# Performance work log

Measured on AMD Instinct MI355X. Metric: run time of the kernel, lower is better.

Reference implementation:

```python
import jax, jax.numpy as jnp
import numpy as np

N, E, L, S = 10000, 200000, 128, 10
NODE_IN, EDGE_IN = 29, 4  # vel_hist(15)+vel_mag(5)+bound(6)+force(3); rel_disp(3)+rel_dist(1)
EPS = 1e-5  # haiku LayerNorm default


def _mlp(x, params):
    # hk.nets.MLP([L]*num_mlp_layers + [out]) with relu activations
    for W, b in params[:-1]:
        x = jax.nn.relu(x @ W + b)
    W, b = params[-1]
    return x @ W + b


def _ln(x, s, o):
    m = jnp.mean(x, axis=-1, keepdims=True)
    v = jnp.mean(jnp.square(x - m), axis=-1, keepdims=True)
    return (x - m) * jax.lax.rsqrt(v + EPS) * s + o


def _init_mlp(key, dims, stack=None):
    Ws, bs = [], []
    for i in range(len(dims) - 1):
        key, k = jax.random.split(key)
        shp = (dims[i], dims[i + 1]) if stack is None else (stack, dims[i], dims[i + 1])
        Ws.append(jax.random.normal(k, shp, jnp.float32) / np.float32(np.sqrt(dims[i])))
        bshp = (dims[i + 1],) if stack is None else (stack, dims[i + 1])
        bs.append(jnp.zeros(bshp, jnp.float32))
    return Ws, bs


def setup_inputs() -> dict:
    key = jax.random.key(0)
    ks = jax.random.split(key, 16)
    inp = {
        'vel_hist': jax.random.normal(ks[0], (N, 15), jnp.float32),
        'vel_mag': jax.random.normal(ks[1], (N, 5), jnp.float32),
        'bound': jax.random.normal(ks[2], (N, 6), jnp.float32),
        'force': jax.random.normal(ks[3], (N, 3), jnp.float32),
        'rel_disp': jax.random.normal(ks[4], (E, 3), jnp.float32),
        'rel_dist': jax.random.normal(ks[5], (E, 1), jnp.float32),
        'senders': jax.random.randint(ks[6], (E,), 0, N, jnp.int32),
        'receivers': jax.random.randint(ks[7], (E,), 0, N, jnp.int32),
    }
    enW, enB = _init_mlp(ks[8], [NODE_IN, L, L, L])
    eeW, eeB = _init_mlp(ks[9], [EDGE_IN, L, L, L])
    peW, peB = _init_mlp(ks[10], [3 * L, L, L, L], stack=S)
    pnW, pnB = _init_mlp(ks[11], [2 * L, L, L, L], stack=S)
    deW, deB = _init_mlp(ks[12], [L, L, L, 3])
    for pre, (Ws, Bs) in [('en', (enW, enB)), ('ee', (eeW, eeB)), ('pe', (peW, peB)), ('pn', (pnW, pnB)), ('de', (deW, deB))]:
        for i in range(3):
            inp[f'{pre}_W{i}'] = Ws[i]
            inp[f'{pre}_b{i}'] = Bs[i]
    inp['en_s'] = jnp.ones((L,), jnp.float32); inp['en_o'] = jnp.zeros((L,), jnp.float32)
    inp['ee_s'] = jnp.ones((L,), jnp.float32); inp['ee_o'] = jnp.zeros((L,), jnp.float32)
    inp['pe_s'] = jnp.ones((S, L), jnp.float32); inp['pe_o'] = jnp.zeros((S, L), jnp.float32)
    inp['pn_s'] = jnp.ones((S, L), jnp.float32); inp['pn_o'] = jnp.zeros((S, L), jnp.float32)
    return inp


def reference(vel_hist, vel_mag, bound, force, rel_disp, rel_dist,
              en_W0, en_b0, en_W1, en_b1, en_W2, en_b2, en_s, en_o,
              ee_W0, ee_b0, ee_W1, ee_b1, ee_W2, ee_b2, ee_s, ee_o,
              pe_W0, pe_b0, pe_W1, pe_b1, pe_W2, pe_b2, pe_s, pe_o,
              pn_W0, pn_b0, pn_W1, pn_b1, pn_W2, pn_b2, pn_s, pn_o,
              de_W0, de_b0, de_W1, de_b1, de_W2, de_b2,
              senders, receivers):
    n = vel_hist.shape[0]
    # encoder
    nodes = _ln(_mlp(jnp.concatenate([vel_hist, vel_mag, bound, force], -1),
                     [(en_W0, en_b0), (en_W1, en_b1), (en_W2, en_b2)]), en_s, en_o)
    edges = _ln(_mlp(jnp.concatenate([rel_disp, rel_dist], -1),
                     [(ee_W0, ee_b0), (ee_W1, ee_b1), (ee_W2, ee_b2)]), ee_s, ee_o)

    # processor: S GraphNetwork blocks with residual adds (distinct params per step)
    def step(carry, p):
        nd, ed = carry
        (W0, b0, W1, b1, W2, b2, s, o, nW0, nb0, nW1, nb1, nW2, nb2, ns, no) = p
        e_in = jnp.concatenate([nd[senders], nd[receivers], ed], -1)  # [E, 3L]
        e_new = _ln(_mlp(e_in, [(W0, b0), (W1, b1), (W2, b2)]), s, o)
        aggr = jax.ops.segment_sum(e_new, receivers, num_segments=n)  # [N, L]
        n_new = _ln(_mlp(jnp.concatenate([nd, aggr], -1), [(nW0, nb0), (nW1, nb1), (nW2, nb2)]), ns, no)
        return (nd + n_new, ed + e_new), None

    (nodes, edges), _ = jax.lax.scan(
        step, (nodes, edges),
        (pe_W0, pe_b0, pe_W1, pe_b1, pe_W2, pe_b2, pe_s, pe_o,
         pn_W0, pn_b0, pn_W1, pn_b1, pn_W2, pn_b2, pn_s, pn_o))

    # decoder (no layer norm)
    return _mlp(nodes, [(de_W0, de_b0), (de_W1, de_b1), (de_W2, de_b2)])
```

## Files before the change

kernel.cpp:

```cpp
#include <hip/hip_runtime.h>

#define NN 10000
#define NE 200000
#define LDIM 128
#define PADB 136
#define NSTEP 10
#define LN_EPS 1e-5f

typedef unsigned short ushort_t;
typedef __attribute__((ext_vector_type(8))) short short8;
typedef __attribute__((ext_vector_type(4))) float f32x4;

#define MFMA16(a, b, c) __builtin_amdgcn_mfma_f32_16x16x32_bf16(a, b, c, 0, 0, 0)

__device__ __forceinline__ ushort_t f2bf(float f) {
  unsigned int u = __float_as_uint(f);
  return (ushort_t)((u + 0x7FFFu + ((u >> 16) & 1u)) >> 16);
}
__device__ __forceinline__ float bf2f(ushort_t h) {
  return __uint_as_float(((unsigned int)h) << 16);
}


#define STAGE_WT(WT, KTOT, K0)                                              \
  {                                                                         \
    const ushort_t* src_ = (WT) + (size_t)(t >> 1) * (KTOT) + (K0) + (t & 1) * 64; \
    ushort_t* dst_ = &Wbuf[(t >> 1) * PADB + (t & 1) * 64];                 \
    _Pragma("unroll")                                                       \
    for (int q_ = 0; q_ < 8; ++q_)                                          \
      *(uint4*)(dst_ + q_ * 8) = *(const uint4*)(src_ + q_ * 8);            \
  }

#define INIT_ACC(BG)                                                        \
  _Pragma("unroll")                                                         \
  for (int nt_ = 0; nt_ < 8; ++nt_) {                                       \
    float bv_ = (BG)[nt_ * 16 + lr];                                        \
    acc[0][nt_] = (f32x4){bv_, bv_, bv_, bv_};                              \
    acc[1][nt_] = acc[0][nt_];                                              \
  }

#define MFMA_K128()                                                         \
  _Pragma("unroll")                                                         \
  for (int ks_ = 0; ks_ < 4; ++ks_) {                                       \
    short8 a0_ = *(const short8*)&Abuf[(rw + lr) * PADB + ks_ * 32 + kg * 8];        \
    short8 a1_ = *(const short8*)&Abuf[(rw + 16 + lr) * PADB + ks_ * 32 + kg * 8];   \
    _Pragma("unroll")                                                       \
    for (int nt_ = 0; nt_ < 8; ++nt_) {                                     \
      short8 b_ = *(const short8*)&Wbuf[(nt_ * 16 + lr) * PADB + ks_ * 32 + kg * 8]; \
      acc[0][nt_] = MFMA16(a0_, b_, acc[0][nt_]);                           \
      acc[1][nt_] = MFMA16(a1_, b_, acc[1][nt_]);                           \
    }                                                                       \
  }

#define RELU_TO_ABUF()                                                      \
  _Pragma("unroll")                                                         \
  for (int mt_ = 0; mt_ < 2; ++mt_) {                                       \
    _Pragma("unroll")                                                       \
    for (int nt_ = 0; nt_ < 8; ++nt_) {                                     \
      _Pragma("unroll")                                                     \
      for (int i_ = 0; i_ < 4; ++i_) {                                      \
        int row_ = rw + 16 * mt_ + kg * 4 + i_;                             \
        Abuf[row_ * PADB + nt_ * 16 + lr] = f2bf(fmaxf(acc[mt_][nt_][i_], 0.f)); \
      }                                                                     \
    }                                                                       \
  }

#define LN_STATS2(MARR, RARR)                                               \
  float MARR[2][4], RARR[2][4];                                             \
  _Pragma("unroll")                                                         \
  for (int mt_ = 0; mt_ < 2; ++mt_) {                                       \
    _Pragma("unroll")                                                       \
    for (int i_ = 0; i_ < 4; ++i_) {                                        \
      float s_ = 0.f;                                                       \
      _Pragma("unroll")                                                     \
      for (int nt_ = 0; nt_ < 8; ++nt_) s_ += acc[mt_][nt_][i_];            \
      s_ += __shfl_xor(s_, 1); s_ += __shfl_xor(s_, 2);                     \
      s_ += __shfl_xor(s_, 4); s_ += __shfl_xor(s_, 8);                     \
      float m_ = s_ * (1.f / 128.f);                                        \
      float v_ = 0.f;                                                       \
      _Pragma("unroll")                                                     \
      for (int nt_ = 0; nt_ < 8; ++nt_) {                                   \
        float d_ = acc[mt_][nt_][i_] - m_; v_ = fmaf(d_, d_, v_);           \
      }                                                                     \
      v_ += __shfl_xor(v_, 1); v_ += __shfl_xor(v_, 2);                     \
      v_ += __shfl_xor(v_, 4); v_ += __shfl_xor(v_, 8);                     \
      MARR[mt_][i_] = m_;                                                   \
      RARR[mt_][i_] = rsqrtf(v_ * (1.f / 128.f) + LN_EPS);                  \
    }                                                                       \
  }

#define LN_TO_FBUF(FB)                                                      \
  _Pragma("unroll")                                                         \
  for (int mt_ = 0; mt_ < 2; ++mt_)                                         \
    _Pragma("unroll")                                                       \
    for (int i_ = 0; i_ < 4; ++i_) {                                        \
      int row_ = rw + 16 * mt_ + kg * 4 + i_;                               \
      _Pragma("unroll")                                                     \
      for (int nt_ = 0; nt_ < 8; ++nt_)                                     \
        (FB)[row_ * 132 + nt_ * 16 + lr] =                                  \
            (acc[mt_][nt_][i_] - lmean[mt_][i_]) * lrstd[mt_][i_] * sv[nt_] + ov[nt_]; \
    }

__global__ void k_prep_w(const float* __restrict__ src, ushort_t* __restrict__ dst,
                         int Ksrc, int Kdst, int N, int steps) {
  const size_t total = (size_t)steps * N * Kdst;
  for (size_t idx = (size_t)blockIdx.x * blockDim.x + threadIdx.x; idx < total;
       idx += (size_t)gridDim.x * blockDim.x) {
    int k = (int)(idx % Kdst);
    size_t tmp = idx / Kdst;
    int n = (int)(tmp % N);
    int s = (int)(tmp / N);
    float v = (k < Ksrc) ? src[((size_t)s * Ksrc + k) * N + n] : 0.f;
    dst[idx] = f2bf(v);
  }
}

__global__ void k_hist(const int* __restrict__ recv, int* __restrict__ cnt) {
  int e = blockIdx.x * 256 + threadIdx.x;
  if (e < NE) atomicAdd(&cnt[recv[e]], 1);
}

__global__ __launch_bounds__(256)
void k_scan(const int* __restrict__ cnt, int* __restrict__ row_start) {
  __shared__ int part[256];
  const int t = threadIdx.x;
  const int base = t * 40;
  int sum = 0;
  for (int i = 0; i < 40; ++i) {
    int b = base + i;
    if (b < NN) sum += cnt[b];
  }
  part[t] = sum;
  __syncthreads();
  for (int off = 1; off < 256; off <<= 1) {
    int v = part[t];
    int u = (t >= off) ? part[t - off] : 0;
    __syncthreads();
    part[t] = v + u;
    __syncthreads();
  }
  int run = (t == 0) ? 0 : part[t - 1];
  for (int i = 0; i < 40; ++i) {
    int b = base + i;
    if (b < NN) { row_start[b] = run; run += cnt[b]; }
  }
  if (t == 255) row_start[NN] = run;
}

__global__ void k_scatter(const int* __restrict__ send, const int* __restrict__ recv,
                          const int* __restrict__ row_start, int* __restrict__ cursor,
                          int* __restrict__ esrc, int* __restrict__ sSend,
                          int* __restrict__ sRecv) {
  int e = blockIdx.x * 256 + threadIdx.x;
  if (e >= NE) return;
  int r = recv[e];
  int pos = row_start[r] + atomicAdd(&cursor[r], 1);
  esrc[pos] = e;
  sSend[pos] = send[e];
  sRecv[pos] = r;
}

__global__ __launch_bounds__(256, 2)
void k_enc_node_m(const float* __restrict__ vh, const float* __restrict__ vm,
                  const float* __restrict__ bd, const float* __restrict__ fc,
                  const ushort_t* __restrict__ Wt0, const float* __restrict__ b0,
                  const ushort_t* __restrict__ Wt1, const float* __restrict__ b1,
                  const ushort_t* __restrict__ Wt2, const float* __restrict__ b2,
                  const float* __restrict__ lns, const float* __restrict__ lno,
                  float* __restrict__ nodes_f, ushort_t* __restrict__ nodes_bf) {
  __shared__ ushort_t Abuf[128 * PADB];
  __shared__ ushort_t Wbuf[128 * PADB];
  const int t = threadIdx.x;
  const int lane = t & 63, wid = t >> 6;
  const int lr = lane & 15, kg = lane >> 4;
  const int rw = wid * 32;
  const int n0 = blockIdx.x * 128;

  for (int idx = t; idx < 128 * 32; idx += 256) {
    int r = idx >> 5, k = idx & 31;
    int ng = n0 + r;
    float v = 0.f;
    if (ng < NN) {
      if (k < 15)      v = vh[(size_t)ng * 15 + k];
      else if (k < 20) v = vm[(size_t)ng * 5 + (k - 15)];
      else if (k < 26) v = bd[(size_t)ng * 6 + (k - 20)];
      else if (k < 29) v = fc[(size_t)ng * 3 + (k - 26)];
    }
    Abuf[r * PADB + k] = f2bf(v);
  }
  {
    const ushort_t* src = Wt0 + (t >> 1) * 32 + (t & 1) * 16;
    ushort_t* dst = &Wbuf[(t >> 1) * PADB + (t & 1) * 16];
    *(uint4*)dst = *(const uint4*)src;
    *(uint4*)(dst + 8) = *(const uint4*)(src + 8);
  }
  f32x4 acc[2][8];
  INIT_ACC(b0)
  __syncthreads();
  {
    short8 a0_ = *(const short8*)&Abuf[(rw + lr) * PADB + kg * 8];
    short8 a1_ = *(const short8*)&Abuf[(rw + 16 + lr) * PADB + kg * 8];
#pragma unroll
    for (int nt_ = 0; nt_ < 8; ++nt_) {
      short8 b_ = *(const short8*)&Wbuf[(nt_ * 16 + lr) * PADB + kg * 8];
      acc[0][nt_] = MFMA16(a0_, b_, acc[0][nt_]);
      acc[1][nt_] = MFMA16(a1_, b_, acc[1][nt_]);
    }
  }
  __syncthreads();
  RELU_TO_ABUF()
  INIT_ACC(b1)
  STAGE_WT(Wt1, 128, 0)
  __syncthreads();
  MFMA_K128()
  __syncthreads();
  RELU_TO_ABUF()
  INIT_ACC(b2)
  STAGE_WT(Wt2, 128, 0)
  __syncthreads();
  MFMA_K128()

  LN_STATS2(lmean, lrstd)
  float sv[8], ov[8];
#pragma unroll
  for (int nt = 0; nt < 8; ++nt) { sv[nt] = lns[nt * 16 + lr]; ov[nt] = lno[nt * 16 + lr]; }
#pragma unroll
  for (int mt = 0; mt < 2; ++mt)
#pragma unroll
    for (int i = 0; i < 4; ++i) {
      int row = rw + 16 * mt + kg * 4 + i;
      int ng = n0 + row;
      if (ng < NN) {
#pragma unroll
        for (int nt = 0; nt < 8; ++nt) {
          float o = (acc[mt][nt][i] - lmean[mt][i]) * lrstd[mt][i] * sv[nt] + ov[nt];
          size_t idx = (size_t)ng * LDIM + nt * 16 + lr;
          nodes_f[idx] = o;
          nodes_bf[idx] = f2bf(o);
        }
      }
    }
}

__global__ __launch_bounds__(256, 2)
void k_enc_edge_m(const float* __restrict__ rel_disp, const float* __restrict__ rel_dist,
                  const int* __restrict__ esrc,
                  const ushort_t* __restrict__ Wt0, const float* __restrict__ b0,
                  const ushort_t* __restrict__ Wt1, const float* __restrict__ b1,
                  const ushort_t* __restrict__ Wt2, const float* __restrict__ b2,
                  const float* __restrict__ lns, const float* __restrict__ lno,
                  float* __restrict__ edges_f) {
  __shared__ ushort_t smem[2 * 128 * PADB];
  __shared__ int eidx[128];
  ushort_t* Abuf = smem;
  ushort_t* Wbuf = smem + 128 * PADB;
  const int t = threadIdx.x;
  const int lane = t & 63, wid = t >> 6;
  const int lr = lane & 15, kg = lane >> 4;
  const int rw = wid * 32;
  const int e0 = blockIdx.x * 128;

  if (t < 128) eidx[t] = (e0 + t < NE) ? esrc[e0 + t] : 0;
  __syncthreads();

  for (int idx = t; idx < 128 * 32; idx += 256) {
    int r = idx >> 5, k = idx & 31;
    float v = 0.f;
    if (e0 + r < NE) {
      int eo = eidx[r];
      if (k < 3)       v = rel_disp[(size_t)eo * 3 + k];
      else if (k == 3) v = rel_dist[eo];
    }
    Abuf[r * PADB + k] = f2bf(v);
  }
  {
    const ushort_t* src = Wt0 + (t >> 1) * 32 + (t & 1) * 16;
    ushort_t* dst = &Wbuf[(t >> 1) * PADB + (t & 1) * 16];
    *(uint4*)dst = *(const uint4*)src;
    *(uint4*)(dst + 8) = *(const uint4*)(src + 8);
  }
  f32x4 acc[2][8];
  INIT_ACC(b0)
  __syncthreads();
  {
    short8 a0_ = *(const short8*)&Abuf[(rw + lr) * PADB + kg * 8];
    short8 a1_ = *(const short8*)&Abuf[(rw + 16 + lr) * PADB + kg * 8];
#pragma unroll
    for (int nt_ = 0; nt_ < 8; ++nt_) {
      short8 b_ = *(const short8*)&Wbuf[(nt_ * 16 + lr) * PADB + kg * 8];
      acc[0][nt_] = MFMA16(a0_, b_, acc[0][nt_]);
      acc[1][nt_] = MFMA16(a1_, b_, acc[1][nt_]);
    }
  }
  __syncthreads();
  RELU_TO_ABUF()
  INIT_ACC(b1)
  STAGE_WT(Wt1, 128, 0)
  __syncthreads();
  MFMA_K128()
  __syncthreads();
  RELU_TO_ABUF()
  INIT_ACC(b2)
  STAGE_WT(Wt2, 128, 0)
  __syncthreads();
  MFMA_K128()

  LN_STATS2(lmean, lrstd)
  float sv[8], ov[8];
#pragma unroll
  for (int nt = 0; nt < 8; ++nt) { sv[nt] = lns[nt * 16 + lr]; ov[nt] = lno[nt * 16 + lr]; }

  float* fbuf = (float*)smem;
  __syncthreads();
  LN_TO_FBUF(fbuf)
  __syncthreads();
#pragma unroll
  for (int q = 0; q < 16; ++q) {
    int F = wid * 4096 + q * 256 + lane * 4;
    int row = F >> 7, col = F & 127;
    if (e0 + row < NE) {
      float4 v = *(const float4*)&fbuf[row * 132 + col];
      *(float4*)&edges_f[(size_t)e0 * LDIM + F] = v;
    }
  }
}

__global__ __launch_bounds__(256, 2)
void k_proc_edge_m(const ushort_t* __restrict__ nodes_bf, float* __restrict__ edges_f,
                   float* __restrict__ aggr,
                   const int* __restrict__ sSend, const int* __restrict__ sRecv,
                   const ushort_t* __restrict__ Wt0, const float* __restrict__ b0,
                   const ushort_t* __restrict__ Wt1, const float* __restrict__ b1,
                   const ushort_t* __restrict__ Wt2, const float* __restrict__ b2,
                   const float* __restrict__ lns, const float* __restrict__ lno) {
  __shared__ ushort_t smem[2 * 128 * PADB];
  __shared__ int sidx[128], ridx[128];
  ushort_t* Abuf = smem;
  ushort_t* Wbuf = smem + 128 * PADB;
  const int t = threadIdx.x;
  const int lane = t & 63, wid = t >> 6;
  const int lr = lane & 15, kg = lane >> 4;
  const int rw = wid * 32;
  const int e0 = blockIdx.x * 128;

  if (t < 128) sidx[t] = (e0 + t < NE) ? sSend[e0 + t] : 0;
  else         ridx[t - 128] = (e0 + t - 128 < NE) ? sRecv[e0 + t - 128] : -1;

  f32x4 acc[2][8];
  float4 eold[16];
  INIT_ACC(b0)
  __syncthreads();

#pragma unroll
  for (int seg = 0; seg < 3; ++seg) {
    if (seg) __syncthreads();
    if (seg < 2) {
      const int r = t >> 1, h = t & 1;
      const int srow = (seg == 0) ? sidx[r] : ((ridx[r] < 0) ? 0 : ridx[r]);
      const ushort_t* src = nodes_bf + (size_t)srow * LDIM + h * 64;
      ushort_t* dst = &Abuf[r * PADB + h * 64];
#pragma unroll
      for (int q = 0; q < 8; ++q)
        *(uint4*)(dst + q * 8) = *(const uint4*)(src + q * 8);
    } else {
#pragma unroll
      for (int q = 0; q < 16; ++q) {
        int F = wid * 4096 + q * 256 + lane * 4;
        int row = F >> 7, col = F & 127;
        float4 v;
        if (e0 + row < NE) v = *(const float4*)&edges_f[(size_t)e0 * LDIM + F];
        else { v.x = v.y = v.z = v.w = 0.f; }
        eold[q] = v;
        ushort4 hv;
        hv.x = f2bf(v.x); hv.y = f2bf(v.y); hv.z = f2bf(v.z); hv.w = f2bf(v.w);
        *(ushort4*)&Abuf[row * PADB + col] = hv;
      }
    }
    STAGE_WT(Wt0, 384, seg * 128)
    __syncthreads();
    MFMA_K128()
  }
  __syncthreads();
  RELU_TO_ABUF()
  INIT_ACC(b1)
  STAGE_WT(Wt1, 128, 0)
  __syncthreads();
  MFMA_K128()
  __syncthreads();
  RELU_TO_ABUF()
  INIT_ACC(b2)
  STAGE_WT(Wt2, 128, 0)
  __syncthreads();
  MFMA_K128()

  LN_STATS2(lmean, lrstd)
  float sv[8], ov[8];
#pragma unroll
  for (int nt = 0; nt < 8; ++nt) { sv[nt] = lns[nt * 16 + lr]; ov[nt] = lno[nt * 16 + lr]; }

  float* fbuf = (float*)smem;
  __syncthreads();
  LN_TO_FBUF(fbuf)
  __syncthreads();

#pragma unroll
  for (int q = 0; q < 16; ++q) {
    int F = wid * 4096 + q * 256 + lane * 4;
    int row = F >> 7, col = F & 127;
    if (e0 + row < NE) {
      float4 nv = *(const float4*)&fbuf[row * 132 + col];
      nv.x += eold[q].x; nv.y += eold[q].y; nv.z += eold[q].z; nv.w += eold[q].w;
      *(float4*)&edges_f[(size_t)e0 * LDIM + F] = nv;
    }
  }

  {
    const int c = t & 127;
    const int half = t >> 7;
    const int r0 = half * 64, r1 = r0 + 64;
    float run = 0.f;
    int cur = ridx[r0];
    for (int r = r0; r < r1; ++r) {
      int rid = ridx[r];
      if (rid != cur) {
        if (cur >= 0) atomicAdd(&aggr[(size_t)cur * LDIM + c], run);
        run = 0.f;
        cur = rid;
      }
      run += fbuf[r * 132 + c];
    }
    if (cur >= 0) atomicAdd(&aggr[(size_t)cur * LDIM + c], run);
  }
}

__global__ __launch_bounds__(256, 2)
void k_proc_node_m(float* __restrict__ nodes_f, ushort_t* __restrict__ nodes_bf,
                   const float* __restrict__ aggr,
                   const ushort_t* __restrict__ Wt0, const float* __restrict__ b0,
                   const ushort_t* __restrict__ Wt1, const float* __restrict__ b1,
                   const ushort_t* __restrict__ Wt2, const float* __restrict__ b2,
                   const float* __restrict__ lns, const float* __restrict__ lno) {
  __shared__ ushort_t Abuf[128 * PADB];
  __shared__ ushort_t Wbuf[128 * PADB];
  const int t = threadIdx.x;
  const int lane = t & 63, wid = t >> 6;
  const int lr = lane & 15, kg = lane >> 4;
  const int rw = wid * 32;
  const int n0 = blockIdx.x * 128;

  f32x4 acc[2][8];
  INIT_ACC(b0)

#pragma unroll
  for (int seg = 0; seg < 2; ++seg) {
    if (seg) __syncthreads();
    {
      const int r = t >> 1, h = t & 1;
      const int ng = n0 + r;
      ushort_t* dst = &Abuf[r * PADB + h * 64];
      if (ng < NN) {
        if (seg == 0) {
          const ushort_t* src = nodes_bf + (size_t)ng * LDIM + h * 64;
#pragma unroll
          for (int q = 0; q < 8; ++q)
            *(uint4*)(dst + q * 8) = *(const uint4*)(src + q * 8);
        } else {
          const float* src = aggr + (size_t)ng * LDIM + h * 64;
#pragma unroll
          for (int q = 0; q < 16; ++q) {
            float4 fv = *(const float4*)(src + q * 4);
            ushort4 hv;
            hv.x = f2bf(fv.x); hv.y = f2bf(fv.y); hv.z = f2bf(fv.z); hv.w = f2bf(fv.w);
            *(ushort4*)(dst + q * 4) = hv;
          }
        }
      } else {
        uint4 z; z.x = z.y = z.z = z.w = 0u;
#pragma unroll
        for (int q = 0; q < 8; ++q) *(uint4*)(dst + q * 8) = z;
      }
    }
    STAGE_WT(Wt0, 256, seg * 128)
    __syncthreads();
    MFMA_K128()
  }
  __syncthreads();
  RELU_TO_ABUF()
  INIT_ACC(b1)
  STAGE_WT(Wt1, 128, 0)
  __syncthreads();
  MFMA_K128()
  __syncthreads();
  RELU_TO_ABUF()
  INIT_ACC(b2)
  STAGE_WT(Wt2, 128, 0)
  __syncthreads();
  MFMA_K128()

  LN_STATS2(lmean, lrstd)
  float sv[8], ov[8];
#pragma unroll
  for (int nt = 0; nt < 8; ++nt) { sv[nt] = lns[nt * 16 + lr]; ov[nt] = lno[nt * 16 + lr]; }
#pragma unroll
  for (int mt = 0; mt < 2; ++mt)
#pragma unroll
    for (int i = 0; i < 4; ++i) {
      int row = rw + 16 * mt + kg * 4 + i;
      int ng = n0 + row;
      if (ng < NN) {
#pragma unroll
        for (int nt = 0; nt < 8; ++nt) {
          float o = (acc[mt][nt][i] - lmean[mt][i]) * lrstd[mt][i] * sv[nt] + ov[nt];
          size_t idx = (size_t)ng * LDIM + nt * 16 + lr;
          float nv = nodes_f[idx] + o;
          nodes_f[idx] = nv;
          nodes_bf[idx] = f2bf(nv);
        }
      }
    }
}

__global__ __launch_bounds__(256, 2)
void k_dec_m(const ushort_t* __restrict__ nodes_bf,
             const ushort_t* __restrict__ Wt0, const float* __restrict__ b0,
             const ushort_t* __restrict__ Wt1, const float* __restrict__ b1,
             const float* __restrict__ W2f, const float* __restrict__ b2,
             float* __restrict__ out) {
  __shared__ ushort_t Abuf[128 * PADB];
  __shared__ ushort_t Wbuf[128 * PADB];
  const int t = threadIdx.x;
  const int lane = t & 63, wid = t >> 6;
  const int lr = lane & 15, kg = lane >> 4;
  const int rw = wid * 32;
  const int n0 = blockIdx.x * 128;

  {
    const int r = t >> 1, h = t & 1;
    const int ng = n0 + r;
    ushort_t* dst = &Abuf[r * PADB + h * 64];
    if (ng < NN) {
      const ushort_t* src = nodes_bf + (size_t)ng * LDIM + h * 64;
#pragma unroll
      for (int q = 0; q < 8; ++q)
        *(uint4*)(dst + q * 8) = *(const uint4*)(src + q * 8);
    } else {
      uint4 z; z.x = z.y = z.z = z.w = 0u;
#pragma unroll
      for (int q = 0; q < 8; ++q) *(uint4*)(dst + q * 8) = z;
    }
  }
  f32x4 acc[2][8];
  INIT_ACC(b0)
  STAGE_WT(Wt0, 128, 0)
  __syncthreads();
  MFMA_K128()
  __syncthreads();
  RELU_TO_ABUF()
  INIT_ACC(b1)
  STAGE_WT(Wt1, 128, 0)
  __syncthreads();
  MFMA_K128()
  __syncthreads();
  RELU_TO_ABUF()
  __syncthreads();

  if (t < 128) {
    const int ng = n0 + t;
    if (ng < NN) {
      float s0 = b2[0], s1 = b2[1], s2 = b2[2];
      for (int k = 0; k < 128; ++k) {
        float xv = bf2f(Abuf[t * PADB + k]);
        s0 = fmaf(xv, W2f[k * 3 + 0], s0);
        s1 = fmaf(xv, W2f[k * 3 + 1], s1);
        s2 = fmaf(xv, W2f[k * 3 + 2], s2);
      }
      out[(size_t)ng * 3 + 0] = s0;
      out[(size_t)ng * 3 + 1] = s1;
      out[(size_t)ng * 3 + 2] = s2;
    }
  }
}

extern "C" void kernel_launch(void* const* d_in, const int* in_sizes, int n_in,
                              void* d_out, int out_size, void* d_ws, size_t ws_size,
                              hipStream_t stream) {
  const float* vel_hist = (const float*)d_in[0];
  const float* vel_mag  = (const float*)d_in[1];
  const float* bnd      = (const float*)d_in[2];
  const float* force    = (const float*)d_in[3];
  const float* rel_disp = (const float*)d_in[4];
  const float* rel_dist = (const float*)d_in[5];
  const int*   senders   = (const int*)d_in[6];
  const int*   receivers = (const int*)d_in[7];
  const float* en_W0 = (const float*)d_in[8];  const float* en_b0 = (const float*)d_in[9];
  const float* en_W1 = (const float*)d_in[10]; const float* en_b1 = (const float*)d_in[11];
  const float* en_W2 = (const float*)d_in[12]; const float* en_b2 = (const float*)d_in[13];
  const float* ee_W0 = (const float*)d_in[14]; const float* ee_b0 = (const float*)d_in[15];
  const float* ee_W1 = (const float*)d_in[16]; const float* ee_b1 = (const float*)d_in[17];
  const float* ee_W2 = (const float*)d_in[18]; const float* ee_b2 = (const float*)d_in[19];
  const float* pe_W0 = (const float*)d_in[20]; const float* pe_b0 = (const float*)d_in[21];
  const float* pe_W1 = (const float*)d_in[22]; const float* pe_b1 = (const float*)d_in[23];
  const float* pe_W2 = (const float*)d_in[24]; const float* pe_b2 = (const float*)d_in[25];
  const float* pn_W0 = (const float*)d_in[26]; const float* pn_b0 = (const float*)d_in[27];
  const float* pn_W1 = (const float*)d_in[28]; const float* pn_b1 = (const float*)d_in[29];
  const float* pn_W2 = (const float*)d_in[30]; const float* pn_b2 = (const float*)d_in[31];
  const float* de_W0 = (const float*)d_in[32]; const float* de_b0 = (const float*)d_in[33];
  const float* de_W1 = (const float*)d_in[34]; const float* de_b1 = (const float*)d_in[35];
  const float* de_W2 = (const float*)d_in[36]; const float* de_b2 = (const float*)d_in[37];
  const float* en_s = (const float*)d_in[38]; const float* en_o = (const float*)d_in[39];
  const float* ee_s = (const float*)d_in[40]; const float* ee_o = (const float*)d_in[41];
  const float* pe_s = (const float*)d_in[42]; const float* pe_o = (const float*)d_in[43];
  const float* pn_s = (const float*)d_in[44]; const float* pn_o = (const float*)d_in[45];

  float* nodes_f = (float*)d_ws;
  float* edges_f = nodes_f + (size_t)NN * LDIM;
  float* aggr    = edges_f + (size_t)NE * LDIM;
  ushort_t* nodes_bf = (ushort_t*)(aggr + (size_t)NN * LDIM);
  ushort_t* w = nodes_bf + (size_t)NN * LDIM;
  ushort_t* wEn0 = w; w += 128 * 32;
  ushort_t* wEn1 = w; w += 128 * 128;
  ushort_t* wEn2 = w; w += 128 * 128;
  ushort_t* wEe0 = w; w += 128 * 32;
  ushort_t* wEe1 = w; w += 128 * 128;
  ushort_t* wEe2 = w; w += 128 * 128;
  ushort_t* wPe0 = w; w += (size_t)NSTEP * 128 * 384;
  ushort_t* wPe1 = w; w += (size_t)NSTEP * 128 * 128;
  ushort_t* wPe2 = w; w += (size_t)NSTEP * 128 * 128;
  ushort_t* wPn0 = w; w += (size_t)NSTEP * 128 * 256;
  ushort_t* wPn1 = w; w += (size_t)NSTEP * 128 * 128;
  ushort_t* wPn2 = w; w += (size_t)NSTEP * 128 * 128;
  ushort_t* wDe0 = w; w += 128 * 128;
  ushort_t* wDe1 = w; w += 128 * 128;
  int* cnt       = (int*)w;
  int* row_start = cnt + NN;
  int* cursor    = row_start + NN + 1;
  int* esrc      = cursor + NN;
  int* sSend     = esrc + NE;
  int* sRecv     = sSend + NE;

  auto prep = [&](const float* src, ushort_t* dst, int Ks, int Kd, int N_, int st) {
    size_t total = (size_t)st * N_ * Kd;
    int blocks = (int)((total + 255) / 256);
    if (blocks > 1024) blocks = 1024;
    k_prep_w<<<blocks, 256, 0, stream>>>(src, dst, Ks, Kd, N_, st);
  };
  prep(en_W0, wEn0, 29, 32, 128, 1);
  prep(en_W1, wEn1, 128, 128, 128, 1);
  prep(en_W2, wEn2, 128, 128, 128, 1);
  prep(ee_W0, wEe0, 4, 32, 128, 1);
  prep(ee_W1, wEe1, 128, 128, 128, 1);
  prep(ee_W2, wEe2, 128, 128, 128, 1);
  prep(pe_W0, wPe0, 384, 384, 128, NSTEP);
  prep(pe_W1, wPe1, 128, 128, 128, NSTEP);
  prep(pe_W2, wPe2, 128, 128, 128, NSTEP);
  prep(pn_W0, wPn0, 256, 256, 128, NSTEP);
  prep(pn_W1, wPn1, 128, 128, 128, NSTEP);
  prep(pn_W2, wPn2, 128, 128, 128, NSTEP);
  prep(de_W0, wDe0, 128, 128, 128, 1);
  prep(de_W1, wDe1, 128, 128, 128, 1);

  hipMemsetAsync(cnt, 0, NN * sizeof(int), stream);
  hipMemsetAsync(cursor, 0, NN * sizeof(int), stream);
  k_hist<<<(NE + 255) / 256, 256, 0, stream>>>(receivers, cnt);
  k_scan<<<1, 256, 0, stream>>>(cnt, row_start);
  k_scatter<<<(NE + 255) / 256, 256, 0, stream>>>(senders, receivers, row_start,
                                                  cursor, esrc, sSend, sRecv);

  const int NB = (NN + 127) / 128;
  const int EB = (NE + 127) / 128;

  k_enc_node_m<<<NB, 256, 0, stream>>>(vel_hist, vel_mag, bnd, force,
      wEn0, en_b0, wEn1, en_b1, wEn2, en_b2, en_s, en_o, nodes_f, nodes_bf);
  k_enc_edge_m<<<EB, 256, 0, stream>>>(rel_disp, rel_dist, esrc,
      wEe0, ee_b0, wEe1, ee_b1, wEe2, ee_b2, ee_s, ee_o, edges_f);

  for (int s = 0; s < NSTEP; ++s) {
    hipMemsetAsync(aggr, 0, (size_t)NN * LDIM * sizeof(float), stream);
    k_proc_edge_m<<<EB, 256, 0, stream>>>(nodes_bf, edges_f, aggr, sSend, sRecv,
        wPe0 + (size_t)s * 128 * 384, pe_b0 + (size_t)s * LDIM,
        wPe1 + (size_t)s * 128 * 128, pe_b1 + (size_t)s * LDIM,
        wPe2 + (size_t)s * 128 * 128, pe_b2 + (size_t)s * LDIM,
        pe_s + (size_t)s * LDIM, pe_o + (size_t)s * LDIM);
    k_proc_node_m<<<NB, 256, 0, stream>>>(nodes_f, nodes_bf, aggr,
        wPn0 + (size_t)s * 128 * 256, pn_b0 + (size_t)s * LDIM,
        wPn1 + (size_t)s * 128 * 128, pn_b1 + (size_t)s * LDIM,
        wPn2 + (size_t)s * 128 * 128, pn_b2 + (size_t)s * LDIM,
        pn_s + (size_t)s * LDIM, pn_o + (size_t)s * LDIM);
  }

  k_dec_m<<<NB, 256, 0, stream>>>(nodes_bf, wDe0, de_b0, wDe1, de_b1, de_W2, de_b2,
                                  (float*)d_out);
}
```

Baseline: 1.750 ms.

## Read weights and gathered node rows directly from global memory in edge MLP

The edge processor kernel no longer stages weights into LDS. MFMA B operands are read straight from global/L2 and A operands for the sender and receiver segments are gathered directly from the node rows. LDS is halved to a single buffer, and the LN output and scatter phase run in two halves so the fbuf fits, which should allow higher occupancy and fewer barriers. The cost is many uncoalesced global loads of weights per wave, which now depend on cache hits, plus an extra synchronisation round in the epilogue.

Result: slower. 2.600 ms (+48.5%).

```diff
diff --git a/kernel.cpp b/kernel.cpp
--- a/kernel.cpp
+++ b/kernel.cpp
@@ -47,6 +47,32 @@
     _Pragma("unroll")                                                       \
     for (int nt_ = 0; nt_ < 8; ++nt_) {                                     \
       short8 b_ = *(const short8*)&Wbuf[(nt_ * 16 + lr) * PADB + ks_ * 32 + kg * 8]; \
+      acc[0][nt_] = MFMA16(a0_, b_, acc[0][nt_]);                           \
+      acc[1][nt_] = MFMA16(a1_, b_, acc[1][nt_]);                           \
+    }                                                                       \
+  }
+
+#define MFMA_K128_GW(WT, KTOT, KOFF)                                        \
+  _Pragma("unroll")                                                         \
+  for (int ks_ = 0; ks_ < 4; ++ks_) {                                       \
+    short8 a0_ = *(const short8*)&Abuf[(rw + lr) * PADB + ks_ * 32 + kg * 8];        \
+    short8 a1_ = *(const short8*)&Abuf[(rw + 16 + lr) * PADB + ks_ * 32 + kg * 8];   \
+    _Pragma("unroll")                                                       \
+    for (int nt_ = 0; nt_ < 8; ++nt_) {                                     \
+      short8 b_ = *(const short8*)&(WT)[(size_t)(nt_ * 16 + lr) * (KTOT) + (KOFF) + ks_ * 32 + kg * 8]; \
+      acc[0][nt_] = MFMA16(a0_, b_, acc[0][nt_]);                           \
+      acc[1][nt_] = MFMA16(a1_, b_, acc[1][nt_]);                           \
+    }                                                                       \
+  }
+
+#define MFMA_K128_GAW(A0P, A1P, WT, KTOT, KOFF)                             \
+  _Pragma("unroll")                                                         \
+  for (int ks_ = 0; ks_ < 4; ++ks_) {                                       \
+    short8 a0_ = *(const short8*)&(A0P)[ks_ * 32 + kg * 8];                 \
+    short8 a1_ = *(const short8*)&(A1P)[ks_ * 32 + kg * 8];                 \
+    _Pragma("unroll")                                                       \
+    for (int nt_ = 0; nt_ < 8; ++nt_) {                                     \
+      short8 b_ = *(const short8*)&(WT)[(size_t)(nt_ * 16 + lr) * (KTOT) + (KOFF) + ks_ * 32 + kg * 8]; \
       acc[0][nt_] = MFMA16(a0_, b_, acc[0][nt_]);                           \
       acc[1][nt_] = MFMA16(a1_, b_, acc[1][nt_]);                           \
     }                                                                       \
@@ -89,18 +115,6 @@
     }                                                                       \
   }
 
-#define LN_TO_FBUF(FB)                                                      \
-  _Pragma("unroll")                                                         \
-  for (int mt_ = 0; mt_ < 2; ++mt_)                                         \
-    _Pragma("unroll")                                                       \
-    for (int i_ = 0; i_ < 4; ++i_) {                                        \
-      int row_ = rw + 16 * mt_ + kg * 4 + i_;                               \
-      _Pragma("unroll")                                                     \
-      for (int nt_ = 0; nt_ < 8; ++nt_)                                     \
-        (FB)[row_ * 132 + nt_ * 16 + lr] =                                  \
-            (acc[mt_][nt_][i_] - lmean[mt_][i_]) * lrstd[mt_][i_] * sv[nt_] + ov[nt_]; \
-    }
-
 __global__ void k_prep_w(const float* __restrict__ src, ushort_t* __restrict__ dst,
                          int Ksrc, int Kdst, int N, int steps) {
   const size_t total = (size_t)steps * N * Kdst;
@@ -312,7 +326,16 @@
 
   float* fbuf = (float*)smem;
   __syncthreads();
-  LN_TO_FBUF(fbuf)
+#pragma unroll
+  for (int mt_ = 0; mt_ < 2; ++mt_)
+#pragma unroll
+    for (int i_ = 0; i_ < 4; ++i_) {
+      int row_ = rw + 16 * mt_ + kg * 4 + i_;
+#pragma unroll
+      for (int nt_ = 0; nt_ < 8; ++nt_)
+        fbuf[row_ * 132 + nt_ * 16 + lr] =
+            (acc[mt_][nt_][i_] - lmean[mt_][i_]) * lrstd[mt_][i_] * sv[nt_] + ov[nt_];
+    }
   __syncthreads();
 #pragma unroll
   for (int q = 0; q < 16; ++q) {
@@ -333,103 +356,117 @@
                    const ushort_t* __restrict__ Wt1, const float* __restrict__ b1,
                    const ushort_t* __restrict__ Wt2, const float* __restrict__ b2,
                    const float* __restrict__ lns, const float* __restrict__ lno) {
-  __shared__ ushort_t smem[2 * 128 * PADB];
-  __shared__ int sidx[128], ridx[128];
-  ushort_t* Abuf = smem;
-  ushort_t* Wbuf = smem + 128 * PADB;
+  __shared__ __align__(16) unsigned char smem[128 * PADB * 2];
+  __shared__ int ridxs[128];
+  ushort_t* Abuf = (ushort_t*)smem;
+  float* fbuf = (float*)smem;
   const int t = threadIdx.x;
   const int lane = t & 63, wid = t >> 6;
   const int lr = lane & 15, kg = lane >> 4;
   const int rw = wid * 32;
   const int e0 = blockIdx.x * 128;
 
-  if (t < 128) sidx[t] = (e0 + t < NE) ? sSend[e0 + t] : 0;
-  else         ridx[t - 128] = (e0 + t - 128 < NE) ? sRecv[e0 + t - 128] : -1;
+  if (t < 128) ridxs[t] = (e0 + t < NE) ? sRecv[e0 + t] : -1;
+
+  const int er0 = e0 + rw + lr, er1 = e0 + rw + 16 + lr;
+  const int s0r = (er0 < NE) ? sSend[er0] : 0;
+  const int s1r = (er1 < NE) ? sSend[er1] : 0;
+  const int r0r = (er0 < NE) ? sRecv[er0] : 0;
+  const int r1r = (er1 < NE) ? sRecv[er1] : 0;
+
+  float4 eold[16];
+#pragma unroll
+  for (int q = 0; q < 16; ++q) {
+    int F = wid * 4096 + q * 256 + lane * 4;
+    int row = F >> 7;
+    if (e0 + row < NE) eold[q] = *(const float4*)&edges_f[(size_t)e0 * LDIM + F];
+    else { eold[q].x = eold[q].y = eold[q].z = eold[q].w = 0.f; }
+  }
 
   f32x4 acc[2][8];
-  float4 eold[16];
   INIT_ACC(b0)
-  __syncthreads();
-
-#pragma unroll
-  for (int seg = 0; seg < 3; ++seg) {
-    if (seg) __syncthreads();
-    if (seg < 2) {
-      const int r = t >> 1, h = t & 1;
-      const int srow = (seg == 0) ? sidx[r] : ((ridx[r] < 0) ? 0 : ridx[r]);
-      const ushort_t* src = nodes_bf + (size_t)srow * LDIM + h * 64;
-      ushort_t* dst = &Abuf[r * PADB + h * 64];
-#pragma unroll
-      for (int q = 0; q < 8; ++q)
-        *(uint4*)(dst + q * 8) = *(const uint4*)(src + q * 8);
-    } else {
+
+  {
+    const ushort_t* a0p = nodes_bf + (size_t)s0r * LDIM;
+    const ushort_t* a1p = nodes_bf + (size_t)s1r * LDIM;
+    MFMA_K128_GAW(a0p, a1p, Wt0, 384, 0)
+  }
+  {
+    const ushort_t* a0p = nodes_bf + (size_t)r0r * LDIM;
+    const ushort_t* a1p = nodes_bf + (size_t)r1r * LDIM;
+    MFMA_K128_GAW(a0p, a1p, Wt0, 384, 128)
+  }
+#pragma unroll
+  for (int q = 0; q < 16; ++q) {
+    int F = wid * 4096 + q * 256 + lane * 4;
+    int row = F >> 7, col = F & 127;
+    ushort4 hv;
+    hv.x = f2bf(eold[q].x); hv.y = f2bf(eold[q].y);
+    hv.z = f2bf(eold[q].z); hv.w = f2bf(eold[q].w);
+    *(ushort4*)&Abuf[row * PADB + col] = hv;
+  }
+  MFMA_K128_GW(Wt0, 384, 256)
+
+  RELU_TO_ABUF()
+  INIT_ACC(b1)
+  MFMA_K128_GW(Wt1, 128, 0)
+  RELU_TO_ABUF()
+  INIT_ACC(b2)
+  MFMA_K128_GW(Wt2, 128, 0)
+
+  LN_STATS2(lmean, lrstd)
+  float sv[8], ov[8];
+#pragma unroll
+  for (int nt = 0; nt < 8; ++nt) { sv[nt] = lns[nt * 16 + lr]; ov[nt] = lno[nt * 16 + lr]; }
+
+  __syncthreads();
+
+#pragma unroll
+  for (int p = 0; p < 2; ++p) {
+    if (p) __syncthreads();
+    if ((wid >> 1) == p) {
+#pragma unroll
+      for (int mt = 0; mt < 2; ++mt)
+#pragma unroll
+        for (int i = 0; i < 4; ++i) {
+          int lrow = (rw - p * 64) + 16 * mt + kg * 4 + i;
+#pragma unroll
+          for (int nt = 0; nt < 8; ++nt)
+            fbuf[lrow * 132 + nt * 16 + lr] =
+                (acc[mt][nt][i] - lmean[mt][i]) * lrstd[mt][i] * sv[nt] + ov[nt];
+        }
+    }
+    __syncthreads();
+    if ((wid >> 1) == p) {
 #pragma unroll
       for (int q = 0; q < 16; ++q) {
         int F = wid * 4096 + q * 256 + lane * 4;
         int row = F >> 7, col = F & 127;
-        float4 v;
-        if (e0 + row < NE) v = *(const float4*)&edges_f[(size_t)e0 * LDIM + F];
-        else { v.x = v.y = v.z = v.w = 0.f; }
-        eold[q] = v;
-        ushort4 hv;
-        hv.x = f2bf(v.x); hv.y = f2bf(v.y); hv.z = f2bf(v.z); hv.w = f2bf(v.w);
-        *(ushort4*)&Abuf[row * PADB + col] = hv;
+        if (e0 + row < NE) {
+          int lrow = row - p * 64;
+          float4 nv = *(const float4*)&fbuf[lrow * 132 + col];
+          nv.x += eold[q].x; nv.y += eold[q].y;
+          nv.z += eold[q].z; nv.w += eold[q].w;
+          *(float4*)&edges_f[(size_t)e0 * LDIM + F] = nv;
+        }
       }
     }
-    STAGE_WT(Wt0, 384, seg * 128)
-    __syncthreads();
-    MFMA_K128()
-  }
-  __syncthreads();
-  RELU_TO_ABUF()
-  INIT_ACC(b1)
-  STAGE_WT(Wt1, 128, 0)
-  __syncthreads();
-  MFMA_K128()
-  __syncthreads();
-  RELU_TO_ABUF()
-  INIT_ACC(b2)
-  STAGE_WT(Wt2, 128, 0)
-  __syncthreads();
-  MFMA_K128()
-
-  LN_STATS2(lmean, lrstd)
-  float sv[8], ov[8];
-#pragma unroll
-  for (int nt = 0; nt < 8; ++nt) { sv[nt] = lns[nt * 16 + lr]; ov[nt] = lno[nt * 16 + lr]; }
-
-  float* fbuf = (float*)smem;
-  __syncthreads();
-  LN_TO_FBUF(fbuf)
-  __syncthreads();
-
-#pragma unroll
-  for (int q = 0; q < 16; ++q) {
-    int F = wid * 4096 + q * 256 + lane * 4;
-    int row = F >> 7, col = F & 127;
-    if (e0 + row < NE) {
-      float4 nv = *(const float4*)&fbuf[row * 132 + col];
-      nv.x += eold[q].x; nv.y += eold[q].y; nv.z += eold[q].z; nv.w += eold[q].w;
-      *(float4*)&edges_f[(size_t)e0 * LDIM + F] = nv;
-    }
-  }
-
-  {
-    const int c = t & 127;
-    const int half = t >> 7;
-    const int r0 = half * 64, r1 = r0 + 64;
-    float run = 0.f;
-    int cur = ridx[r0];
-    for (int r = r0; r < r1; ++r) {
-      int rid = ridx[r];
-      if (rid != cur) {
-        if (cur >= 0) atomicAdd(&aggr[(size_t)cur * LDIM + c], run);
-        run = 0.f;
-        cur = rid;
+    {
+      const int c = t & 127, sub = t >> 7;
+      const int rA = p * 64 + sub * 32, rB = rA + 32;
+      float run = 0.f;
+      int cur = ridxs[rA];
+      for (int r = rA; r < rB; ++r) {
+        int rid = ridxs[r];
+        if (rid != cur) {
+          if (cur >= 0) atomicAdd(&aggr[(size_t)cur * LDIM + c], run);
+          run = 0.f;
+          cur = rid;
+        }
+        run += fbuf[(r - p * 64) * 132 + c];
       }
-      run += fbuf[r * 132 + c];
-    }
-    if (cur >= 0) atomicAdd(&aggr[(size_t)cur * LDIM + c], run);
+      if (cur >= 0) atomicAdd(&aggr[(size_t)cur * LDIM + c], run);
+    }
   }
 }
 
```
